# Performance work log

Hardware: AMD Instinct MI355X
Metric: run time of the kernel (lower is better)

Reference implementation:

```python
import jax, jax.numpy as jnp
import numpy as np

N_NODES = 50000
N_EDGES = 800000
NODE_DIM = 32
EDGE_DIM = 16
HID = 64
MSG_HID = 128
NUM_GRAPHS = 512
NUM_MP = 3
S2S_STEPS = 6


def _lin(k, fan_in, fan_out):
    # torch Linear default init: U(-1/sqrt(fan_in), 1/sqrt(fan_in))
    bound = 1.0 / np.sqrt(fan_in)
    kw, kb = jax.random.split(k)
    W = jax.random.uniform(kw, (fan_in, fan_out), jnp.float32, -bound, bound)
    b = jax.random.uniform(kb, (fan_out,), jnp.float32, -bound, bound)
    return W, b


def setup_inputs() -> dict:
    key = jax.random.key(0)
    ks = jax.random.split(key, 16)
    x_feat = jax.random.normal(ks[0], (N_NODES, NODE_DIM), jnp.float32)
    edge_index = jax.random.randint(ks[1], (2, N_EDGES), 0, N_NODES)
    edge_attr = jax.random.normal(ks[2], (N_EDGES, EDGE_DIM), jnp.float32)
    batch = jnp.sort(jax.random.randint(ks[3], (N_NODES,), 0, NUM_GRAPHS))
    W_emb, b_emb = _lin(ks[4], NODE_DIM, HID)
    W_m1, b_m1 = _lin(ks[5], 2 * HID + EDGE_DIM, MSG_HID)
    W_m2, b_m2 = _lin(ks[6], MSG_HID, HID)
    bnd = 1.0 / np.sqrt(HID)
    gru_W_ih = jax.random.uniform(ks[7], (3 * HID, HID), jnp.float32, -bnd, bnd)
    gru_W_hh = jax.random.uniform(ks[8], (3 * HID, HID), jnp.float32, -bnd, bnd)
    gru_b_ih = jax.random.uniform(ks[9], (3 * HID,), jnp.float32, -bnd, bnd)
    gru_b_hh = jax.random.uniform(ks[9], (3 * HID,), jnp.float32, -bnd, bnd)
    lstm_W_ih = jax.random.uniform(ks[10], (4 * HID, 2 * HID), jnp.float32, -bnd, bnd)
    lstm_W_hh = jax.random.uniform(ks[11], (4 * HID, HID), jnp.float32, -bnd, bnd)
    lstm_b_ih = jax.random.uniform(ks[12], (4 * HID,), jnp.float32, -bnd, bnd)
    lstm_b_hh = jax.random.uniform(ks[12], (4 * HID,), jnp.float32, -bnd, bnd)
    W_r1, b_r1 = _lin(ks[13], 2 * HID, HID)
    W_r2, b_r2 = _lin(ks[14], HID, 1)
    return dict(x_feat=x_feat, edge_index=edge_index, edge_attr=edge_attr, batch=batch,
                W_emb=W_emb, b_emb=b_emb, W_m1=W_m1, b_m1=b_m1, W_m2=W_m2, b_m2=b_m2,
                gru_W_ih=gru_W_ih, gru_W_hh=gru_W_hh, gru_b_ih=gru_b_ih, gru_b_hh=gru_b_hh,
                lstm_W_ih=lstm_W_ih, lstm_W_hh=lstm_W_hh, lstm_b_ih=lstm_b_ih, lstm_b_hh=lstm_b_hh,
                W_r1=W_r1, b_r1=b_r1, W_r2=W_r2, b_r2=b_r2)


def reference(x_feat, edge_index, edge_attr, batch,
              W_emb, b_emb, W_m1, b_m1, W_m2, b_m2,
              gru_W_ih, gru_W_hh, gru_b_ih, gru_b_hh,
              lstm_W_ih, lstm_W_hh, lstm_b_ih, lstm_b_hh,
              W_r1, b_r1, W_r2, b_r2):
    src, dst = edge_index[0], edge_index[1]
    x = x_feat @ W_emb + b_emb  # [N, HID]
    h = x  # GRU hidden state (seq_len=1 GRU)
    for _ in range(NUM_MP):
        # message: cat([x_i (target), x_j (source), edge_attr]) -> MLP -> scatter-add to target
        mi = jnp.concatenate([x[dst], x[src], edge_attr], axis=-1)  # [E, 2H+Ed]
        msg = jnp.maximum(mi @ W_m1 + b_m1, 0.0) @ W_m2 + b_m2  # [E, H]
        m = jax.ops.segment_sum(msg, dst, num_segments=N_NODES)  # [N, H]
        # torch GRU cell, gate order (r, z, n)
        gi = m @ gru_W_ih.T + gru_b_ih
        gh = h @ gru_W_hh.T + gru_b_hh
        ir, iz, i_n = jnp.split(gi, 3, axis=-1)
        hr, hz, h_n = jnp.split(gh, 3, axis=-1)
        r = jax.nn.sigmoid(ir + hr)
        z = jax.nn.sigmoid(iz + hz)
        n = jnp.tanh(i_n + r * h_n)
        h = (1.0 - z) * n + z * h
        x = h
    # Set2Set pooling
    qh = jnp.zeros((NUM_GRAPHS, HID), x.dtype)
    qc = jnp.zeros((NUM_GRAPHS, HID), x.dtype)
    q_star = jnp.zeros((NUM_GRAPHS, 2 * HID), x.dtype)
    for _ in range(S2S_STEPS):
        # torch LSTM cell, gate order (i, f, g, o)
        g = q_star @ lstm_W_ih.T + lstm_b_ih + qh @ lstm_W_hh.T + lstm_b_hh
        gi_, gf, gg, go = jnp.split(g, 4, axis=-1)
        qc = jax.nn.sigmoid(gf) * qc + jax.nn.sigmoid(gi_) * jnp.tanh(gg)
        qh = jax.nn.sigmoid(go) * jnp.tanh(qc)
        e = jnp.sum(x * qh[batch], axis=-1)  # [N]
        emax = jax.ops.segment_max(e, batch, num_segments=NUM_GRAPHS)
        a = jnp.exp(e - emax[batch])
        asum = jax.ops.segment_sum(a, batch, num_segments=NUM_GRAPHS)
        a = a / asum[batch]  # segment softmax
        rvec = jax.ops.segment_sum(a[:, None] * x, batch, num_segments=NUM_GRAPHS)  # [B, H]
        q_star = jnp.concatenate([qh, rvec], axis=-1)
    out = jnp.maximum(q_star @ W_r1 + b_r1, 0.0) @ W_r2 + b_r2
    return out
```

## Files before the change

kernel.cpp:

```cpp
#include <hip/hip_runtime.h>
#include <hip/hip_bf16.h>

#define HID 64
#define MSG 128
#define NDIM 32
#define EDIM 16
#define NG 512
#define SCAP 192

typedef unsigned short u16;
typedef unsigned int u32;
typedef _Float16 h8 __attribute__((ext_vector_type(8)));
typedef _Float16 h4 __attribute__((ext_vector_type(4)));
typedef _Float16 h2 __attribute__((ext_vector_type(2)));

__device__ __forceinline__ u16 f2b(float f){union{float f;u32 i;}v;v.f=f;u32 r=v.i+0x7FFF+((v.i>>16)&1);return (u16)(r>>16);}
__device__ __forceinline__ u32 pack2(float a,float b){return (u32)f2b(a)|((u32)f2b(b)<<16);}
__device__ __forceinline__ float blo(u32 w){union{u32 i;float f;}v;v.i=w<<16;return v.f;}
__device__ __forceinline__ float bhi(u32 w){union{u32 i;float f;}v;v.i=w&0xffff0000u;return v.f;}
__device__ __forceinline__ float sigm(float x){return 1.0f/(1.0f+expf(-x));}
__device__ __forceinline__ int rfl(int x){return __builtin_amdgcn_readfirstlane(x);}

__global__ void k_hist(const int* __restrict__ idx, int n, int* __restrict__ cnt) {
    int i = blockIdx.x * blockDim.x + threadIdx.x;
    int stride = gridDim.x * blockDim.x;
    for (; i < n; i += stride) atomicAdd(&cnt[idx[i]], 1);
}

__global__ void k_scanA(const int* __restrict__ in, int* __restrict__ out,
                        int* __restrict__ bsum, int n) {
    __shared__ int sh[1024];
    int i = blockIdx.x * 1024 + threadIdx.x;
    int v = (i < n) ? in[i] : 0;
    sh[threadIdx.x] = v;
    __syncthreads();
    for (int off = 1; off < 1024; off <<= 1) {
        int t = (threadIdx.x >= off) ? sh[threadIdx.x - off] : 0;
        __syncthreads();
        sh[threadIdx.x] += t;
        __syncthreads();
    }
    if (i < n) out[i] = sh[threadIdx.x] - v;
    if (threadIdx.x == 1023) bsum[blockIdx.x] = sh[1023];
}
__global__ void k_scanB(const int* __restrict__ bsum, int* __restrict__ boff, int nb) {
    if (threadIdx.x == 0) {
        int r = 0;
        for (int b = 0; b < nb; b++) { boff[b] = r; r += bsum[b]; }
        boff[nb] = r;
    }
}
__global__ void k_scanC(int* __restrict__ out, const int* __restrict__ boff, int n, int nb) {
    int i = blockIdx.x * blockDim.x + threadIdx.x;
    if (i < n) out[i] += boff[i >> 10];
    else if (i == n) out[n] = boff[nb];
}

__global__ void k_gptr(const int* __restrict__ batch, int N, int* __restrict__ gptr) {
    int g = blockIdx.x * blockDim.x + threadIdx.x;
    if (g > NG) return;
    int lo = 0, hi = N;
    while (lo < hi) { int mid = (lo + hi) >> 1; if (batch[mid] < g) lo = mid + 1; else hi = mid; }
    gptr[g] = lo;
}

__global__ void k_scatter(const int* __restrict__ src, const int* __restrict__ dst, int n,
                          const int* __restrict__ ptr, int* __restrict__ cursor,
                          int* __restrict__ eidx, int* __restrict__ slist) {
    int i = blockIdx.x * blockDim.x + threadIdx.x;
    int stride = gridDim.x * blockDim.x;
    for (; i < n; i += stride) {
        int d = dst[i];
        int pos = ptr[d] + atomicAdd(&cursor[d], 1);
        eidx[pos] = i;
        slist[pos] = src[i];
    }
}

__global__ void k_permea(const int* __restrict__ eidx, const float* __restrict__ ea,
                         _Float16* __restrict__ eap, int E) {
    int i = blockIdx.x * blockDim.x + threadIdx.x;
    if (i >= E) return;
    int e = eidx[i];
    const float* s = ea + (size_t)e * EDIM;
    float4 a = *(const float4*)s, b = *(const float4*)(s + 4);
    float4 c = *(const float4*)(s + 8), d = *(const float4*)(s + 12);
    h8 o0, o1;
    o0[0]=(_Float16)a.x; o0[1]=(_Float16)a.y; o0[2]=(_Float16)a.z; o0[3]=(_Float16)a.w;
    o0[4]=(_Float16)b.x; o0[5]=(_Float16)b.y; o0[6]=(_Float16)b.z; o0[7]=(_Float16)b.w;
    o1[0]=(_Float16)c.x; o1[1]=(_Float16)c.y; o1[2]=(_Float16)c.z; o1[3]=(_Float16)c.w;
    o1[4]=(_Float16)d.x; o1[5]=(_Float16)d.y; o1[6]=(_Float16)d.z; o1[7]=(_Float16)d.w;
    h8* dp = (h8*)(eap + (size_t)i * EDIM);
    dp[0] = o0; dp[1] = o1;
}

__global__ void k_packw(const float* __restrict__ Wih, const float* __restrict__ Whh,
                        uint2* __restrict__ gWa, u32* __restrict__ gWb) {
    int t = blockIdx.x * blockDim.x + threadIdx.x;
    if (t < 64 * 64) {
        int k = t >> 6, c = t & 63;
        gWa[t] = make_uint2(pack2(Wih[c * 64 + k], Wih[(64 + c) * 64 + k]),
                            pack2(Wih[(128 + c) * 64 + k], Whh[c * 64 + k]));
        gWb[t] = pack2(Whh[(64 + c) * 64 + k], Whh[(128 + c) * 64 + k]);
    }
}

__global__ void k_packl(const float* __restrict__ lWih, const float* __restrict__ lWhh,
                        float* __restrict__ WT1, float* __restrict__ WT2) {
    int t = blockIdx.x * blockDim.x + threadIdx.x;
    if (t < 256 * 128) { int g = t >> 7, k = t & 127; WT1[k * 256 + g] = lWih[g * 128 + k]; }
    if (t < 256 * 64)  { int g = t >> 6, k = t & 63;  WT2[k * 256 + g] = lWhh[g * 64 + k]; }
}

__global__ void k_embed(const float* __restrict__ xf, const float* __restrict__ We,
                        const float* __restrict__ be, float* __restrict__ xh, int N) {
    __shared__ float Wl[NDIM * HID];
    for (int t = threadIdx.x; t < NDIM * HID; t += blockDim.x) Wl[t] = We[t];
    __syncthreads();
    int total = N * HID;
    int stride = gridDim.x * blockDim.x;
    for (int idx = blockIdx.x * blockDim.x + threadIdx.x; idx < total; idx += stride) {
        int n = idx >> 6, c = idx & 63;
        const float* xr = xf + n * NDIM;
        float acc = be[c];
#pragma unroll
        for (int k = 0; k < NDIM; k++) acc += xr[k] * Wl[k * HID + c];
        xh[idx] = acc;
    }
}

__global__ void __launch_bounds__(256)
k_prep(const float* __restrict__ xh, const float* __restrict__ Wm1,
       const float* __restrict__ bm1, float* __restrict__ Hb,
       _Float16* __restrict__ PsH, int N) {
    __shared__ float Wl[64 * 256];
    for (int t = threadIdx.x; t < 64 * 256; t += 256) {
        int k = t >> 8, cc = t & 255;
        Wl[t] = (cc < 128) ? Wm1[k * 128 + cc] : Wm1[(64 + k) * 128 + (cc - 128)];
    }
    __syncthreads();
    int wv = threadIdx.x >> 6, lane = threadIdx.x & 63;
    int cc = lane * 4;
    float4 bias;
    if (lane < 32) bias = *(const float4*)&bm1[cc];
    else bias = make_float4(0.f, 0.f, 0.f, 0.f);
    int ngroups = (N + 7) >> 3;
    for (int g = blockIdx.x * 4 + wv; g < ngroups; g += gridDim.x * 4) {
        int base = rfl(g) * 8;
        const float* xp[8];
#pragma unroll
        for (int t = 0; t < 8; t++) {
            int d = base + t; if (d > N - 1) d = N - 1;
            xp[t] = xh + (size_t)d * 64;
        }
        float4 acc[8];
#pragma unroll
        for (int t = 0; t < 8; t++) acc[t] = bias;
#pragma unroll 2
        for (int k4 = 0; k4 < 16; k4++) {
            int k = k4 * 4;
            float4 xv4[8];
#pragma unroll
            for (int t = 0; t < 8; t++) xv4[t] = *(const float4*)&xp[t][k];
#pragma unroll
            for (int kk = 0; kk < 4; kk++) {
                float4 w = *(const float4*)&Wl[(k + kk) * 256 + cc];
#pragma unroll
                for (int t = 0; t < 8; t++) {
                    float xv = kk == 0 ? xv4[t].x : kk == 1 ? xv4[t].y : kk == 2 ? xv4[t].z : xv4[t].w;
                    acc[t].x += xv * w.x; acc[t].y += xv * w.y;
                    acc[t].z += xv * w.z; acc[t].w += xv * w.w;
                }
            }
        }
#pragma unroll
        for (int t = 0; t < 8; t++) {
            int d = base + t;
            if (d < N) {
                if (lane < 32) *(float4*)&Hb[(size_t)d * 128 + cc] = acc[t];
                else {
                    h4 o;
                    o[0] = (_Float16)acc[t].x; o[1] = (_Float16)acc[t].y;
                    o[2] = (_Float16)acc[t].z; o[3] = (_Float16)acc[t].w;
                    *(h4*)&PsH[(size_t)d * 128 + (cc - 128)] = o;
                }
            }
        }
    }
}

__global__ void __launch_bounds__(256)
k_edge(const _Float16* __restrict__ PsH, const _Float16* __restrict__ eap,
       const float* __restrict__ Wm1, const int* __restrict__ ptr,
       const int* __restrict__ slist, float* __restrict__ Hb, int N) {
    int c = threadIdx.x & 127;
    int half = threadIdx.x >> 7;
    h2 wh[8];
#pragma unroll
    for (int k = 0; k < 8; k++) {
        h2 t;
        t[0] = (_Float16)Wm1[128 * 128 + (2 * k) * 128 + c];
        t[1] = (_Float16)Wm1[128 * 128 + (2 * k + 1) * 128 + c];
        wh[k] = t;
    }
    for (int dd = blockIdx.x * 2 + half; dd < N; dd += gridDim.x * 2) {
        int d = rfl(dd);
        float pd = Hb[(size_t)d * 128 + c];
        int eb = rfl(ptr[d]), ee = rfl(ptr[d + 1]);
        const int* sp = slist + eb;
        const _Float16* ep = eap + (size_t)eb * EDIM;
        int ne = ee - eb;
        float acc = 0.f;
        int i = 0;
        for (; i + 8 <= ne; i += 8) {
            int ns[8];
#pragma unroll
            for (int j = 0; j < 8; j++) ns[j] = rfl(sp[i + j]);
            float pv[8];
#pragma unroll
            for (int j = 0; j < 8; j++) pv[j] = (float)PsH[(size_t)ns[j] * 128 + c];
#pragma unroll
            for (int j = 0; j < 8; j++) {
                union { uint4 u; h2 h[4]; } A, B;
                A.u = *(const uint4*)(ep + (size_t)(i + j) * EDIM);
                B.u = *(const uint4*)(ep + (size_t)(i + j) * EDIM + 8);
                float pe = 0.f;
#pragma unroll
                for (int k = 0; k < 4; k++) pe = __builtin_amdgcn_fdot2(A.h[k], wh[k], pe, false);
#pragma unroll
                for (int k = 0; k < 4; k++) pe = __builtin_amdgcn_fdot2(B.h[k], wh[4 + k], pe, false);
                acc += fmaxf(pd + pv[j] + pe, 0.f);
            }
        }
        for (; i < ne; i++) {
            int n0 = rfl(sp[i]);
            float pv = (float)PsH[(size_t)n0 * 128 + c];
            union { uint4 u; h2 h[4]; } A, B;
            A.u = *(const uint4*)(ep + (size_t)i * EDIM);
            B.u = *(const uint4*)(ep + (size_t)i * EDIM + 8);
            float pe = 0.f;
#pragma unroll
            for (int k = 0; k < 4; k++) pe = __builtin_amdgcn_fdot2(A.h[k], wh[k], pe, false);
#pragma unroll
            for (int k = 0; k < 4; k++) pe = __builtin_amdgcn_fdot2(B.h[k], wh[4 + k], pe, false);
            acc += fmaxf(pd + pv + pe, 0.f);
        }
        Hb[(size_t)d * 128 + c] = acc;
    }
}

__global__ void __launch_bounds__(256)
k_msg(const float* __restrict__ H, const float* __restrict__ Wm2,
      const float* __restrict__ bm2, const int* __restrict__ ptr,
      float* __restrict__ m, int N) {
    __shared__ float W2[128 * 64];
    for (int t = threadIdx.x; t < 128 * 64; t += 256) W2[t] = Wm2[t];
    __syncthreads();
    int wv = threadIdx.x >> 6, lane = threadIdx.x & 63;
    float b2 = bm2[lane];
    int ngroups = (N + 3) >> 2;
    for (int g = blockIdx.x * 4 + wv; g < ngroups; g += gridDim.x * 4) {
        int base = rfl(g) * 4;
        const float* hp[4];
#pragma unroll
        for (int t = 0; t < 4; t++) { int d = base + t; if (d > N - 1) d = N - 1; hp[t] = H + (size_t)d * 128; }
        float acc[4] = {0.f, 0.f, 0.f, 0.f};
#pragma unroll 2
        for (int k4 = 0; k4 < 32; k4++) {
            int k = k4 * 4;
            float4 h4v[4];
#pragma unroll
            for (int t = 0; t < 4; t++) h4v[t] = *(const float4*)&hp[t][k];
#pragma unroll
            for (int kk = 0; kk < 4; kk++) {
                float w = W2[(k + kk) * 64 + lane];
#pragma unroll
                for (int t = 0; t < 4; t++) {
                    float hv = kk == 0 ? h4v[t].x : kk == 1 ? h4v[t].y : kk == 2 ? h4v[t].z : h4v[t].w;
                    acc[t] += hv * w;
                }
            }
        }
#pragma unroll
        for (int t = 0; t < 4; t++) {
            int d = base + t;
            if (d < N) {
                float deg = (float)(ptr[d + 1] - ptr[d]);
                m[(size_t)d * 64 + lane] = acc[t] + deg * b2;
            }
        }
    }
}

__global__ void __launch_bounds__(256)
k_gru(const float* __restrict__ m, const uint2* __restrict__ gWa,
      const u32* __restrict__ gWb, const float* __restrict__ bih,
      const float* __restrict__ bhh, float* __restrict__ xh, int N) {
    __shared__ uint2 Wa[64 * 64];
    __shared__ u32 Wb[64 * 64];
    {
        const uint4* s1 = (const uint4*)gWa;
        uint4* d1 = (uint4*)Wa;
        for (int t = threadIdx.x; t < 2048; t += 256) d1[t] = s1[t];
        const uint4* s2 = (const uint4*)gWb;
        uint4* d2 = (uint4*)Wb;
        for (int t = threadIdx.x; t < 1024; t += 256) d2[t] = s2[t];
    }
    __syncthreads();
    int wv = threadIdx.x >> 6, lane = threadIdx.x & 63;
    float br = bih[lane], bz = bih[64 + lane], bn = bih[128 + lane];
    float cr = bhh[lane], cz = bhh[64 + lane], cn = bhh[128 + lane];
    for (int dd = blockIdx.x * 4 + wv; dd < N; dd += gridDim.x * 4) {
        int d = rfl(dd);
        const float* mp = m + (size_t)d * 64;
        const float* hp = xh + (size_t)d * 64;
        float hv = hp[lane];
        float gir = br, giz = bz, gin = bn, ghr = cr, ghz = cz, ghn = cn;
#pragma unroll 2
        for (int k4 = 0; k4 < 16; k4++) {
            int k = k4 * 4;
            float4 m4 = *(const float4*)&mp[k];
            float4 h4v = *(const float4*)&hp[k];
#pragma unroll
            for (int kk = 0; kk < 4; kk++) {
                uint2 wa = Wa[(k + kk) * 64 + lane];
                u32 wb = Wb[(k + kk) * 64 + lane];
                float mk = kk == 0 ? m4.x : kk == 1 ? m4.y : kk == 2 ? m4.z : m4.w;
                float hk = kk == 0 ? h4v.x : kk == 1 ? h4v.y : kk == 2 ? h4v.z : h4v.w;
                gir += mk * blo(wa.x); giz += mk * bhi(wa.x); gin += mk * blo(wa.y);
                ghr += hk * bhi(wa.y); ghz += hk * blo(wb); ghn += hk * bhi(wb);
            }
        }
        float r = sigm(gir + ghr);
        float z = sigm(giz + ghz);
        float nn = tanhf(gin + r * ghn);
        xh[(size_t)d * 64 + lane] = (1.f - z) * nn + z * hv;
    }
}

__global__ void __launch_bounds__(1024)
k_s2s(const float* __restrict__ xh, const int* __restrict__ gptr,
      const float* __restrict__ WT1, const float* __restrict__ WT2,
      const float* __restrict__ lbih, const float* __restrict__ lbhh,
      const float* __restrict__ Wr1, const float* __restrict__ br1,
      const float* __restrict__ Wr2, const float* __restrict__ br2,
      float* __restrict__ out) {
    int b = blockIdx.x, tid = threadIdx.x;
    __shared__ float xl[SCAP * 64];
    __shared__ float qs[128], qhl[64], qcs[64], g[256], red[16], asums[16], rvs[1024];
    int start = gptr[b], end = gptr[b + 1];
    int seg = end - start;
    bool uselds = (seg <= SCAP);
    if (uselds) {
        int tot = seg * 64;
        for (int t = tid; t < tot; t += 1024) xl[t] = xh[(size_t)start * 64 + t];
    }
    if (tid < 128) qs[tid] = 0.f;
    if (tid < 64) { qhl[tid] = 0.f; qcs[tid] = 0.f; }
    __syncthreads();
    int grp = tid >> 6, lane = tid & 63;
    int gate = tid & 255, part = tid >> 8;
    for (int s = 0; s < 6; s++) {
        {
            float acc = 0.f;
            int k0 = part * 32;
#pragma unroll 8
            for (int k = k0; k < k0 + 32; k++) acc += qs[k] * WT1[k * 256 + gate];
            int k1 = part * 16;
#pragma unroll 8
            for (int k = k1; k < k1 + 16; k++) acc += qhl[k] * WT2[k * 256 + gate];
            rvs[tid] = acc;
        }
        __syncthreads();
        if (tid < 256) g[tid] = lbih[tid] + lbhh[tid] + rvs[tid] + rvs[256 + tid] + rvs[512 + tid] + rvs[768 + tid];
        __syncthreads();
        if (tid < 64) {
            float ig = sigm(g[tid]), fg = sigm(g[64 + tid]);
            float gg = tanhf(g[128 + tid]), og = sigm(g[192 + tid]);
            float c = fg * qcs[tid] + ig * gg;
            float h = og * tanhf(c);
            qcs[tid] = c; qhl[tid] = h; qs[tid] = h;
        }
        __syncthreads();
        float qv = qhl[lane];
        float mloc = -3.4e38f, asl = 0.f, rv = 0.f;
        for (int n = grp; n < seg; n += 16) {
            float xv = uselds ? xl[n * 64 + lane] : xh[(size_t)(start + n) * 64 + lane];
            float p = xv * qv;
#pragma unroll
            for (int off = 32; off > 0; off >>= 1) p += __shfl_xor(p, off);
            float mnew = fmaxf(mloc, p);
            float corr = expf(mloc - mnew);
            float a = expf(p - mnew);
            asl = asl * corr + a;
            rv = rv * corr + a * xv;
            mloc = mnew;
        }
        if (lane == 0) red[grp] = mloc;
        __syncthreads();
        float gmax = red[0];
#pragma unroll
        for (int j = 1; j < 16; j++) gmax = fmaxf(gmax, red[j]);
        float sc = expf(mloc - gmax);
        rvs[tid] = rv * sc;
        if (lane == 0) asums[grp] = asl * sc;
        __syncthreads();
        if (tid < 64) {
            float rt = 0.f, at = 0.f;
#pragma unroll
            for (int j = 0; j < 16; j++) { rt += rvs[tid + 64 * j]; at += asums[j]; }
            qs[64 + tid] = (at > 0.f) ? rt / at : 0.f;
        }
        __syncthreads();
    }
    if (tid < 64) {
        float a2 = br1[tid];
#pragma unroll 8
        for (int k = 0; k < 128; k++) a2 += qs[k] * Wr1[k * 64 + tid];
        a2 = fmaxf(a2, 0.f);
        float v = a2 * Wr2[tid];
#pragma unroll
        for (int off = 32; off > 0; off >>= 1) v += __shfl_xor(v, off);
        if (tid == 0) out[b] = v + br2[0];
    }
}

extern "C" void kernel_launch(void* const* d_in, const int* in_sizes, int n_in,
                              void* d_out, int out_size, void* d_ws, size_t ws_size,
                              hipStream_t stream) {
    const float* x_feat = (const float*)d_in[0];
    const int*   ei     = (const int*)d_in[1];
    const float* eattr  = (const float*)d_in[2];
    const int*   batch  = (const int*)d_in[3];
    const float* W_emb  = (const float*)d_in[4];
    const float* b_emb  = (const float*)d_in[5];
    const float* W_m1   = (const float*)d_in[6];
    const float* b_m1   = (const float*)d_in[7];
    const float* W_m2   = (const float*)d_in[8];
    const float* b_m2   = (const float*)d_in[9];
    const float* gWih   = (const float*)d_in[10];
    const float* gWhh   = (const float*)d_in[11];
    const float* gbih   = (const float*)d_in[12];
    const float* gbhh   = (const float*)d_in[13];
    const float* lWih   = (const float*)d_in[14];
    const float* lWhh   = (const float*)d_in[15];
    const float* lbih   = (const float*)d_in[16];
    const float* lbhh   = (const float*)d_in[17];
    const float* Wr1    = (const float*)d_in[18];
    const float* br1    = (const float*)d_in[19];
    const float* Wr2    = (const float*)d_in[20];
    const float* br2    = (const float*)d_in[21];

    int N = in_sizes[0] / NDIM;
    int E = in_sizes[1] / 2;

    char* w = (char*)d_ws;
    auto alloc = [&](size_t b) { char* p = w; w += (b + 511) & ~(size_t)511; return p; };
    float*     xh    = (float*)alloc((size_t)N * 64 * 4);
    _Float16*  PsH   = (_Float16*)alloc((size_t)N * 128 * 2);
    float*     Hb    = (float*)alloc((size_t)N * 128 * 4);
    int*       ptr   = (int*)alloc((size_t)(N + 1) * 4);
    int*       slist = (int*)alloc((size_t)E * 4);
    _Float16*  eap   = (_Float16*)alloc((size_t)E * EDIM * 2);
    uint2*     gWa   = (uint2*)alloc((size_t)4096 * 8);
    u32*       gWb   = (u32*)alloc((size_t)4096 * 4);
    float*     WT1   = (float*)alloc((size_t)128 * 256 * 4);
    float*     WT2   = (float*)alloc((size_t)64 * 256 * 4);
    int*       gptr  = (int*)alloc((size_t)(NG + 1) * 4);
    int*       bsum  = (int*)alloc(128 * 4);
    int*       boff  = (int*)alloc(128 * 4);
    char* z0 = w;
    int*       cnt    = (int*)alloc((size_t)N * 4);
    int*       cursor = (int*)alloc((size_t)N * 4);
    char* z0e = w;
    char*      mbase = alloc((size_t)N * 64 * 4);
    float*     mb    = (float*)mbase;
    int*       eidx  = (int*)mbase;

    hipMemsetAsync(z0, 0, (size_t)(z0e - z0), stream);

    int NB = (N + 1023) / 1024;
    k_hist<<<1024, 256, 0, stream>>>(ei + E, E, cnt);
    k_scanA<<<NB, 1024, 0, stream>>>(cnt, ptr, bsum, N);
    k_scanB<<<1, 64, 0, stream>>>(bsum, boff, NB);
    k_scanC<<<(N + 256) / 256, 256, 0, stream>>>(ptr, boff, N, NB);
    k_gptr<<<3, 256, 0, stream>>>(batch, N, gptr);
    k_scatter<<<3125, 256, 0, stream>>>(ei, ei + E, E, ptr, cursor, eidx, slist);
    k_permea<<<(E + 255) / 256, 256, 0, stream>>>(eidx, eattr, eap, E);
    k_packw<<<16, 256, 0, stream>>>(gWih, gWhh, gWa, gWb);
    k_packl<<<128, 256, 0, stream>>>(lWih, lWhh, WT1, WT2);

    k_embed<<<2048, 256, 0, stream>>>(x_feat, W_emb, b_emb, xh, N);

    for (int r = 0; r < 3; r++) {
        k_prep<<<391, 256, 0, stream>>>(xh, W_m1, b_m1, Hb, PsH, N);
        k_edge<<<4096, 256, 0, stream>>>(PsH, eap, W_m1, ptr, slist, Hb, N);
        k_msg<<<1024, 256, 0, stream>>>(Hb, W_m2, b_m2, ptr, mb, N);
        k_gru<<<1280, 256, 0, stream>>>(mb, gWa, gWb, gbih, gbhh, xh, N);
    }
    k_s2s<<<NG, 1024, 0, stream>>>(xh, gptr, WT1, WT2, lbih, lbhh,
                                   Wr1, br1, Wr2, br2, (float*)d_out);
}
```

Baseline: 1.044 ms.

## Fold message second linear into GRU input weights and fuse msg+GRU kernels

Precomputes the product of W_m2 and the GRU input weights (plus a folded bias scaled by degree), so the separate message kernel and its 64-wide intermediate buffer are eliminated. A single node kernel reads the 128-wide aggregated hidden directly and computes GRU gates with fp16 dot2 instructions, using weights staged in 72KB of dynamic shared memory. The node state now ping-pongs between two buffers because the fused kernel reads x while writing the new x. Trades a larger K (128 vs 64) for the input gate matmul and fp16 weight/activation precision for fewer launches and less memory traffic.

```diff
diff --git a/kernel.cpp b/kernel.cpp
--- a/kernel.cpp
+++ b/kernel.cpp
@@ -14,12 +14,20 @@
 typedef _Float16 h4 __attribute__((ext_vector_type(4)));
 typedef _Float16 h2 __attribute__((ext_vector_type(2)));
 
-__device__ __forceinline__ u16 f2b(float f){union{float f;u32 i;}v;v.f=f;u32 r=v.i+0x7FFF+((v.i>>16)&1);return (u16)(r>>16);}
-__device__ __forceinline__ u32 pack2(float a,float b){return (u32)f2b(a)|((u32)f2b(b)<<16);}
-__device__ __forceinline__ float blo(u32 w){union{u32 i;float f;}v;v.i=w<<16;return v.f;}
-__device__ __forceinline__ float bhi(u32 w){union{u32 i;float f;}v;v.i=w&0xffff0000u;return v.f;}
 __device__ __forceinline__ float sigm(float x){return 1.0f/(1.0f+expf(-x));}
 __device__ __forceinline__ int rfl(int x){return __builtin_amdgcn_readfirstlane(x);}
+__device__ __forceinline__ u32 pkh(float a, float b){
+    union { h2 h; u32 u; } v; v.h[0] = (_Float16)a; v.h[1] = (_Float16)b; return v.u;
+}
+__device__ __forceinline__ h2 pk2h(float a, float b){
+    union { __fp16 __attribute__((ext_vector_type(2))) r; h2 h; } v;
+    v.r = __builtin_amdgcn_cvt_pkrtz(a, b);
+    return v.h;
+}
+__device__ __forceinline__ float fdot2_(h2 a, u32 w, float c){
+    union { u32 u; h2 h; } v; v.u = w;
+    return __builtin_amdgcn_fdot2(a, v.h, c, false);
+}
 
 __global__ void k_hist(const int* __restrict__ idx, int n, int* __restrict__ cnt) {
     int i = blockIdx.x * blockDim.x + threadIdx.x;
@@ -94,14 +102,51 @@
     dp[0] = o0; dp[1] = o1;
 }
 
-__global__ void k_packw(const float* __restrict__ Wih, const float* __restrict__ Whh,
-                        uint2* __restrict__ gWa, u32* __restrict__ gWb) {
+__global__ void k_fuse(const float* __restrict__ Wih, const float* __restrict__ Whh,
+                       const float* __restrict__ W2, const float* __restrict__ bm2,
+                       uint4* __restrict__ gGA, uint2* __restrict__ gGB,
+                       uint4* __restrict__ gUA, uint2* __restrict__ gUB,
+                       float* __restrict__ gbb) {
     int t = blockIdx.x * blockDim.x + threadIdx.x;
-    if (t < 64 * 64) {
-        int k = t >> 6, c = t & 63;
-        gWa[t] = make_uint2(pack2(Wih[c * 64 + k], Wih[(64 + c) * 64 + k]),
-                            pack2(Wih[(128 + c) * 64 + k], Whh[c * 64 + k]));
-        gWb[t] = pack2(Whh[(64 + c) * 64 + k], Whh[(128 + c) * 64 + k]);
+    if (t < 2048) {
+        int k4 = t >> 6, c = t & 63;
+        float G[3][4];
+#pragma unroll
+        for (int g = 0; g < 3; g++)
+#pragma unroll
+            for (int kk = 0; kk < 4; kk++) {
+                int j = 4 * k4 + kk;
+                const float* w2r = W2 + (size_t)j * 64;
+                const float* wir = Wih + (size_t)(g * 64 + c) * 64;
+                float s = 0.f;
+                for (int k = 0; k < 64; k++) s += w2r[k] * wir[k];
+                G[g][kk] = s;
+            }
+        uint4 A; uint2 B;
+        A.x = pkh(G[0][0], G[0][1]); A.y = pkh(G[1][0], G[1][1]);
+        A.z = pkh(G[2][0], G[2][1]); A.w = pkh(G[0][2], G[0][3]);
+        B.x = pkh(G[1][2], G[1][3]); B.y = pkh(G[2][2], G[2][3]);
+        gGA[t] = A; gGB[t] = B;
+    } else if (t < 3072) {
+        int u = t - 2048;
+        int k4 = u >> 6, c = u & 63;
+        float U[3][4];
+#pragma unroll
+        for (int g = 0; g < 3; g++)
+#pragma unroll
+            for (int kk = 0; kk < 4; kk++)
+                U[g][kk] = Whh[(size_t)(g * 64 + c) * 64 + 4 * k4 + kk];
+        uint4 A; uint2 B;
+        A.x = pkh(U[0][0], U[0][1]); A.y = pkh(U[1][0], U[1][1]);
+        A.z = pkh(U[2][0], U[2][1]); A.w = pkh(U[0][2], U[0][3]);
+        B.x = pkh(U[1][2], U[1][3]); B.y = pkh(U[2][2], U[2][3]);
+        gUA[u] = A; gUB[u] = B;
+    } else if (t < 3072 + 192) {
+        int cg = t - 3072;
+        const float* wir = Wih + (size_t)cg * 64;
+        float s = 0.f;
+        for (int k = 0; k < 64; k++) s += bm2[k] * wir[k];
+        gbb[cg] = s;
     }
 }
 
@@ -250,91 +295,52 @@
 }
 
 __global__ void __launch_bounds__(256)
-k_msg(const float* __restrict__ H, const float* __restrict__ Wm2,
-      const float* __restrict__ bm2, const int* __restrict__ ptr,
-      float* __restrict__ m, int N) {
-    __shared__ float W2[128 * 64];
-    for (int t = threadIdx.x; t < 128 * 64; t += 256) W2[t] = Wm2[t];
+k_node(const float* __restrict__ H, const uint4* __restrict__ gGA, const uint2* __restrict__ gGB,
+       const uint4* __restrict__ gUA, const uint2* __restrict__ gUB,
+       const float* __restrict__ gbb, const float* __restrict__ bih, const float* __restrict__ bhh,
+       const int* __restrict__ ptr, const float* __restrict__ xin, float* __restrict__ xout, int N) {
+    extern __shared__ char smem[];
+    uint4* GA = (uint4*)smem;
+    uint2* GB = (uint2*)(smem + 32768);
+    uint4* UA = (uint4*)(smem + 49152);
+    uint2* UB = (uint2*)(smem + 65536);
+    for (int t = threadIdx.x; t < 2048; t += 256) { GA[t] = gGA[t]; GB[t] = gGB[t]; }
+    for (int t = threadIdx.x; t < 1024; t += 256) { UA[t] = gUA[t]; UB[t] = gUB[t]; }
     __syncthreads();
     int wv = threadIdx.x >> 6, lane = threadIdx.x & 63;
-    float b2 = bm2[lane];
-    int ngroups = (N + 3) >> 2;
-    for (int g = blockIdx.x * 4 + wv; g < ngroups; g += gridDim.x * 4) {
-        int base = rfl(g) * 4;
-        const float* hp[4];
-#pragma unroll
-        for (int t = 0; t < 4; t++) { int d = base + t; if (d > N - 1) d = N - 1; hp[t] = H + (size_t)d * 128; }
-        float acc[4] = {0.f, 0.f, 0.f, 0.f};
-#pragma unroll 2
-        for (int k4 = 0; k4 < 32; k4++) {
-            int k = k4 * 4;
-            float4 h4v[4];
-#pragma unroll
-            for (int t = 0; t < 4; t++) h4v[t] = *(const float4*)&hp[t][k];
-#pragma unroll
-            for (int kk = 0; kk < 4; kk++) {
-                float w = W2[(k + kk) * 64 + lane];
-#pragma unroll
-                for (int t = 0; t < 4; t++) {
-                    float hv = kk == 0 ? h4v[t].x : kk == 1 ? h4v[t].y : kk == 2 ? h4v[t].z : h4v[t].w;
-                    acc[t] += hv * w;
-                }
-            }
-        }
-#pragma unroll
-        for (int t = 0; t < 4; t++) {
-            int d = base + t;
-            if (d < N) {
-                float deg = (float)(ptr[d + 1] - ptr[d]);
-                m[(size_t)d * 64 + lane] = acc[t] + deg * b2;
-            }
-        }
-    }
-}
-
-__global__ void __launch_bounds__(256)
-k_gru(const float* __restrict__ m, const uint2* __restrict__ gWa,
-      const u32* __restrict__ gWb, const float* __restrict__ bih,
-      const float* __restrict__ bhh, float* __restrict__ xh, int N) {
-    __shared__ uint2 Wa[64 * 64];
-    __shared__ u32 Wb[64 * 64];
-    {
-        const uint4* s1 = (const uint4*)gWa;
-        uint4* d1 = (uint4*)Wa;
-        for (int t = threadIdx.x; t < 2048; t += 256) d1[t] = s1[t];
-        const uint4* s2 = (const uint4*)gWb;
-        uint4* d2 = (uint4*)Wb;
-        for (int t = threadIdx.x; t < 1024; t += 256) d2[t] = s2[t];
-    }
-    __syncthreads();
-    int wv = threadIdx.x >> 6, lane = threadIdx.x & 63;
+    float gbr = gbb[lane], gbz = gbb[64 + lane], gbn = gbb[128 + lane];
     float br = bih[lane], bz = bih[64 + lane], bn = bih[128 + lane];
     float cr = bhh[lane], cz = bhh[64 + lane], cn = bhh[128 + lane];
     for (int dd = blockIdx.x * 4 + wv; dd < N; dd += gridDim.x * 4) {
         int d = rfl(dd);
-        const float* mp = m + (size_t)d * 64;
-        const float* hp = xh + (size_t)d * 64;
-        float hv = hp[lane];
-        float gir = br, giz = bz, gin = bn, ghr = cr, ghz = cz, ghn = cn;
+        const float* hp = H + (size_t)d * 128;
+        const float* xp = xin + (size_t)d * 64;
+        float hv = xp[lane];
+        float deg = (float)(ptr[d + 1] - ptr[d]);
+        float gr = br + deg * gbr, gz = bz + deg * gbz, gn = bn + deg * gbn;
+#pragma unroll 2
+        for (int k4 = 0; k4 < 32; k4++) {
+            float4 hx = *(const float4*)&hp[k4 * 4];
+            h2 a01 = pk2h(hx.x, hx.y), a23 = pk2h(hx.z, hx.w);
+            uint4 wa = GA[k4 * 64 + lane];
+            uint2 wb = GB[k4 * 64 + lane];
+            gr = fdot2_(a01, wa.x, gr); gz = fdot2_(a01, wa.y, gz); gn = fdot2_(a01, wa.z, gn);
+            gr = fdot2_(a23, wa.w, gr); gz = fdot2_(a23, wb.x, gz); gn = fdot2_(a23, wb.y, gn);
+        }
+        float hr_ = cr, hz_ = cz, hn_ = cn;
 #pragma unroll 2
         for (int k4 = 0; k4 < 16; k4++) {
-            int k = k4 * 4;
-            float4 m4 = *(const float4*)&mp[k];
-            float4 h4v = *(const float4*)&hp[k];
-#pragma unroll
-            for (int kk = 0; kk < 4; kk++) {
-                uint2 wa = Wa[(k + kk) * 64 + lane];
-                u32 wb = Wb[(k + kk) * 64 + lane];
-                float mk = kk == 0 ? m4.x : kk == 1 ? m4.y : kk == 2 ? m4.z : m4.w;
-                float hk = kk == 0 ? h4v.x : kk == 1 ? h4v.y : kk == 2 ? h4v.z : h4v.w;
-                gir += mk * blo(wa.x); giz += mk * bhi(wa.x); gin += mk * blo(wa.y);
-                ghr += hk * bhi(wa.y); ghz += hk * blo(wb); ghn += hk * bhi(wb);
-            }
-        }
-        float r = sigm(gir + ghr);
-        float z = sigm(giz + ghz);
-        float nn = tanhf(gin + r * ghn);
-        xh[(size_t)d * 64 + lane] = (1.f - z) * nn + z * hv;
+            float4 hx = *(const float4*)&xp[k4 * 4];
+            h2 a01 = pk2h(hx.x, hx.y), a23 = pk2h(hx.z, hx.w);
+            uint4 wa = UA[k4 * 64 + lane];
+            uint2 wb = UB[k4 * 64 + lane];
+            hr_ = fdot2_(a01, wa.x, hr_); hz_ = fdot2_(a01, wa.y, hz_); hn_ = fdot2_(a01, wa.z, hn_);
+            hr_ = fdot2_(a23, wa.w, hr_); hz_ = fdot2_(a23, wb.x, hz_); hn_ = fdot2_(a23, wb.y, hn_);
+        }
+        float r = sigm(gr + hr_);
+        float z = sigm(gz + hz_);
+        float nn = tanhf(gn + r * hn_);
+        xout[(size_t)d * 64 + lane] = (1.f - z) * nn + z * hv;
     }
 }
 
@@ -457,13 +463,18 @@
     char* w = (char*)d_ws;
     auto alloc = [&](size_t b) { char* p = w; w += (b + 511) & ~(size_t)511; return p; };
     float*     xh    = (float*)alloc((size_t)N * 64 * 4);
+    float*     xh2   = (float*)alloc((size_t)N * 64 * 4);
     _Float16*  PsH   = (_Float16*)alloc((size_t)N * 128 * 2);
     float*     Hb    = (float*)alloc((size_t)N * 128 * 4);
     int*       ptr   = (int*)alloc((size_t)(N + 1) * 4);
     int*       slist = (int*)alloc((size_t)E * 4);
+    int*       eidx  = (int*)alloc((size_t)E * 4);
     _Float16*  eap   = (_Float16*)alloc((size_t)E * EDIM * 2);
-    uint2*     gWa   = (uint2*)alloc((size_t)4096 * 8);
-    u32*       gWb   = (u32*)alloc((size_t)4096 * 4);
+    uint4*     gGA   = (uint4*)alloc((size_t)2048 * 16);
+    uint2*     gGB   = (uint2*)alloc((size_t)2048 * 8);
+    uint4*     gUA   = (uint4*)alloc((size_t)1024 * 16);
+    uint2*     gUB   = (uint2*)alloc((size_t)1024 * 8);
+    float*     gbb   = (float*)alloc((size_t)192 * 4);
     float*     WT1   = (float*)alloc((size_t)128 * 256 * 4);
     float*     WT2   = (float*)alloc((size_t)64 * 256 * 4);
     int*       gptr  = (int*)alloc((size_t)(NG + 1) * 4);
@@ -473,11 +484,12 @@
     int*       cnt    = (int*)alloc((size_t)N * 4);
     int*       cursor = (int*)alloc((size_t)N * 4);
     char* z0e = w;
-    char*      mbase = alloc((size_t)N * 64 * 4);
-    float*     mb    = (float*)mbase;
-    int*       eidx  = (int*)mbase;
 
     hipMemsetAsync(z0, 0, (size_t)(z0e - z0), stream);
+
+    hipError_t attr_err = hipFuncSetAttribute((const void*)k_node,
+        hipFuncAttributeMaxDynamicSharedMemorySize, 73728);
+    (void)attr_err;
 
     int NB = (N + 1023) / 1024;
     k_hist<<<1024, 256, 0, stream>>>(ei + E, E, cnt);
@@ -487,17 +499,20 @@
     k_gptr<<<3, 256, 0, stream>>>(batch, N, gptr);
     k_scatter<<<3125, 256, 0, stream>>>(ei, ei + E, E, ptr, cursor, eidx, slist);
     k_permea<<<(E + 255) / 256, 256, 0, stream>>>(eidx, eattr, eap, E);
-    k_packw<<<16, 256, 0, stream>>>(gWih, gWhh, gWa, gWb);
+    k_fuse<<<13, 256, 0, stream>>>(gWih, gWhh, W_m2, b_m2, gGA, gGB, gUA, gUB, gbb);
     k_packl<<<128, 256, 0, stream>>>(lWih, lWhh, WT1, WT2);
 
     k_embed<<<2048, 256, 0, stream>>>(x_feat, W_emb, b_emb, xh, N);
 
+    float* xa = xh;
+    float* xb = xh2;
     for (int r = 0; r < 3; r++) {
-        k_prep<<<391, 256, 0, stream>>>(xh, W_m1, b_m1, Hb, PsH, N);
+        k_prep<<<391, 256, 0, stream>>>(xa, W_m1, b_m1, Hb, PsH, N);
         k_edge<<<4096, 256, 0, stream>>>(PsH, eap, W_m1, ptr, slist, Hb, N);
-        k_msg<<<1024, 256, 0, stream>>>(Hb, W_m2, b_m2, ptr, mb, N);
-        k_gru<<<1280, 256, 0, stream>>>(mb, gWa, gWb, gbih, gbhh, xh, N);
-    }
-    k_s2s<<<NG, 1024, 0, stream>>>(xh, gptr, WT1, WT2, lbih, lbhh,
+        k_node<<<512, 256, 73728, stream>>>(Hb, gGA, gGB, gUA, gUB, gbb, gbih, gbhh,
+                                            ptr, xa, xb, N);
+        float* t = xa; xa = xb; xb = t;
+    }
+    k_s2s<<<NG, 1024, 0, stream>>>(xa, gptr, WT1, WT2, lbih, lbhh,
                                    Wr1, br1, Wr2, br2, (float*)d_out);
 }
```

After: 1.071 ms. 2.6% more time.
